# Kernel tuning notes

Hardware: AMD Instinct MI355X
Metric: run time of the kernel (lower is better)

The kernel has to match this reference:

```python
import jax, jax.numpy as jnp
from jax import lax
import numpy as np

V, E, H = 32000, 32, 8  # vocab, embed dim, hidden dim
S, B = 128, 64          # seq_len, batch


def setup_inputs() -> dict:
    key = jax.random.key(0)
    ks = jax.random.split(key, 16)
    u = lambda k, shape, s: jax.random.uniform(k, shape, jnp.float32, -s, s)
    sH = 1.0 / np.sqrt(H)
    sE = 1.0 / np.sqrt(E)
    sV = 1.0 / np.sqrt(V)
    return {
        "input_batch": jax.random.randint(ks[0], (S, B), 0, V),
        "lookup": u(ks[1], (V, E), sE),
        "weight_xf": u(ks[2], (E, H), sH),
        "weight_hf": u(ks[3], (H, H), sH),
        "weight_xb": u(ks[4], (E, H), sH),
        "weight_hb": u(ks[5], (H, H), sH),
        "weight_o": u(ks[6], (2 * H, V), sV),
        "H_f": u(ks[7], (H,), sH),
        "H_b": u(ks[8], (H,), sH),
        "b_f1": u(ks[9], (H,), sH),
        "b_f2": u(ks[10], (H,), sH),
        "b_b1": u(ks[11], (H,), sH),
        "b_b2": u(ks[12], (H,), sH),
        "b_o": u(ks[13], (V,), sV),
    }


def reference(input_batch, lookup, weight_xf, weight_hf, weight_xb, weight_hb,
              weight_o, H_f, H_b, b_f1, b_f2, b_b1, b_b2, b_o):
    seq, bsz = input_batch.shape
    X = lookup[input_batch]  # [S, B, E]

    # NOTE: the torch code stores the hidden state BEFORE consuming token i
    # (H_f_table[i] = Hf_pre), so scan emits the carry before the update.
    def step_f(h, x):
        h_new = jnp.tanh(x @ weight_xf + b_f1 + h @ weight_hf + b_f2)
        return h_new, h

    def step_b(h, x):
        h_new = jnp.tanh(x @ weight_xb + b_b1 + h @ weight_hb + b_b2)
        return h_new, h

    h0f = jnp.broadcast_to(H_f, (bsz, H))
    h0b = jnp.broadcast_to(H_b, (bsz, H))
    _, Hf_table = lax.scan(step_f, h0f, X)            # [S, B, H] (pre-states)
    _, Hb_rev = lax.scan(step_b, h0b, X[::-1])        # reversed pre-states
    Hb_table = Hb_rev[::-1]                           # [S, B, H]

    Hcat = jnp.concatenate([Hf_table, Hb_table], axis=-1)   # [S, B, 2H]
    logits = jnp.einsum('sbh,hv->sbv', Hcat, weight_o) + b_o
    return jax.nn.log_softmax(logits, axis=-1)
```

## Files before the change

kernel.cpp:

```cpp
#include <hip/hip_runtime.h>

#define SEQ 128
#define BSZ 64
#define EMB 32
#define HD  8
#define VOC 32000
#define NPOS (SEQ * BSZ)
#define NRB  (NPOS / 32)
#define NVS  40
#define TPW  25

typedef float f32x4  __attribute__((ext_vector_type(4)));
typedef short bf16x8 __attribute__((ext_vector_type(8)));
typedef float f32x16 __attribute__((ext_vector_type(16)));

__device__ __forceinline__ unsigned short f2bf(float f) {
    union { float f; unsigned int u; } x; x.f = f;
    unsigned int r = x.u + 0x7fffu + ((x.u >> 16) & 1u);
    return (unsigned short)(r >> 16);
}

__global__ __launch_bounds__(256) void xproj_kernel(
    const int*   __restrict__ idx,
    const float* __restrict__ lookup,
    const float* __restrict__ Wxf, const float* __restrict__ Wxb,
    const float* __restrict__ bf1, const float* __restrict__ bf2,
    const float* __restrict__ bb1, const float* __restrict__ bb2,
    float* __restrict__ xpf, float* __restrict__ xpb)
{
    const int i = blockIdx.x * 256 + threadIdx.x;
    if (i >= NPOS) return;
    const int s = i >> 6;
    const int b = i & 63;

    const float* xr = lookup + (size_t)idx[i] * EMB;
    float x[EMB];
#pragma unroll
    for (int e = 0; e < EMB; ++e) x[e] = xr[e];

#pragma unroll
    for (int h = 0; h < HD; ++h) {
        float af = bf1[h] + bf2[h];
        float ab = bb1[h] + bb2[h];
#pragma unroll
        for (int e = 0; e < EMB; ++e) {
            af = fmaf(x[e], Wxf[e * HD + h], af);
            ab = fmaf(x[e], Wxb[e * HD + h], ab);
        }
        xpf[(b * HD + h) * SEQ + s]             = af;
        xpb[(b * HD + h) * SEQ + (SEQ - 1 - s)] = ab;
    }
}

__global__ __launch_bounds__(512) void rnn_scan_kernel(
    const float* __restrict__ xpf, const float* __restrict__ xpb,
    const float* __restrict__ Whf, const float* __restrict__ Whb,
    const float* __restrict__ Hf0, const float* __restrict__ Hb0,
    unsigned short* __restrict__ hc2)
{
    const int dir = blockIdx.x;
    const int tid = threadIdx.x;
    const int b   = tid >> 3;
    const int h   = tid & 7;

    const float* Wh = dir ? Whb : Whf;
    const float* xp = (dir ? xpb : xpf) + (size_t)tid * SEQ;

    float wh[HD];
#pragma unroll
    for (int j = 0; j < HD; ++j) wh[j] = Wh[j * HD + h];

    float xs[SEQ];
    const f32x4* xp4 = (const f32x4*)xp;
#pragma unroll
    for (int q = 0; q < SEQ / 4; ++q) {
        f32x4 v = xp4[q];
        xs[4 * q + 0] = v.x; xs[4 * q + 1] = v.y;
        xs[4 * q + 2] = v.z; xs[4 * q + 3] = v.w;
    }

    float hcur = dir ? Hb0[h] : Hf0[h];
    const int koff = dir ? HD : 0;

#pragma unroll
    for (int t = 0; t < SEQ; ++t) {
        const int s = dir ? (SEQ - 1 - t) : t;
        hc2[(s * BSZ + b) * 16 + koff + h] = f2bf(hcur);

        float acc = xs[t];
#pragma unroll
        for (int j = 0; j < HD; ++j)
            acc = fmaf(__shfl(hcur, j, 8), wh[j], acc);

        float e = __expf(2.0f * acc);
        hcur = (e - 1.0f) / (e + 1.0f);
    }
}

__global__ __launch_bounds__(256) void wo_prep_kernel(
    const float* __restrict__ Wo, unsigned short* __restrict__ wt)
{
    const int v = blockIdx.x * 256 + threadIdx.x;
    if (v >= VOC) return;
#pragma unroll
    for (int k = 0; k < 16; ++k)
        wt[v * 16 + k] = f2bf(Wo[k * VOC + v]);
}

__global__ __launch_bounds__(256) void lse_partial_kernel(
    const unsigned short* __restrict__ hc2,
    const unsigned short* __restrict__ wt,
    const float* __restrict__ bo,
    float* __restrict__ partial)
{
    const int gw   = blockIdx.x * 4 + (threadIdx.x >> 6);
    const int rb   = gw / NVS;
    const int vs   = gw - rb * NVS;
    const int lane = threadIdx.x & 63;
    const int half = lane >> 5;
    const int lc   = lane & 31;

    const bf16x8 afrag = *(const bf16x8*)(hc2 + (size_t)(rb * 32 + lc) * 16 + half * 8);

    f32x16 zv;
#pragma unroll
    for (int i = 0; i < 16; ++i) zv[i] = 0.0f;

    float sacc[16];
#pragma unroll
    for (int g = 0; g < 16; ++g) sacc[g] = 0.0f;

    for (int t = 0; t < TPW; ++t) {
        const int v0 = (vs * TPW + t) * 32;
        const bf16x8 bfrag = *(const bf16x8*)(wt + (size_t)(v0 + lc) * 16 + half * 8);
        f32x16 d = __builtin_amdgcn_mfma_f32_32x32x16_bf16(afrag, bfrag, zv, 0, 0, 0);
        const float bov = bo[v0 + lc];
#pragma unroll
        for (int g = 0; g < 16; ++g)
            sacc[g] += __expf(d[g] + bov);
    }

#pragma unroll
    for (int g = 0; g < 16; ++g) {
        float s = sacc[g];
        s += __shfl_xor(s, 1, 32);
        s += __shfl_xor(s, 2, 32);
        s += __shfl_xor(s, 4, 32);
        s += __shfl_xor(s, 8, 32);
        s += __shfl_xor(s, 16, 32);
        sacc[g] = s;
    }

    if (lc == 0) {
#pragma unroll
        for (int g = 0; g < 16; ++g) {
            const int row = (g & 3) + 8 * (g >> 2) + 4 * half;
            partial[(size_t)(rb * 32 + row) * NVS + vs] = sacc[g];
        }
    }
}

__global__ __launch_bounds__(256) void lse_reduce_kernel(
    const float* __restrict__ partial, float* __restrict__ lse)
{
    const int row = blockIdx.x * 256 + threadIdx.x;
    if (row >= NPOS) return;
    const f32x4* p4 = (const f32x4*)(partial + (size_t)row * NVS);
    float s = 0.0f;
#pragma unroll
    for (int q = 0; q < NVS / 4; ++q) {
        f32x4 v = p4[q];
        s += v.x + v.y + v.z + v.w;
    }
    lse[row] = logf(s);
}

__global__ __launch_bounds__(256) void out_mfma_kernel(
    const unsigned short* __restrict__ hc2,
    const unsigned short* __restrict__ wt,
    const float* __restrict__ bo,
    const float* __restrict__ lse,
    float* __restrict__ out)
{
    const int gw   = blockIdx.x * 4 + (threadIdx.x >> 6);
    const int rb   = gw / NVS;
    const int vs   = gw - rb * NVS;
    const int lane = threadIdx.x & 63;
    const int half = lane >> 5;
    const int lc   = lane & 31;

    const bf16x8 afrag = *(const bf16x8*)(hc2 + (size_t)(rb * 32 + lc) * 16 + half * 8);

    f32x16 zv;
#pragma unroll
    for (int i = 0; i < 16; ++i) zv[i] = 0.0f;

    float lse16[16];
#pragma unroll
    for (int g = 0; g < 16; ++g) {
        const int row = (g & 3) + 8 * (g >> 2) + 4 * half;
        lse16[g] = lse[rb * 32 + row];
    }

    for (int t = 0; t < TPW; ++t) {
        const int v0 = (vs * TPW + t) * 32;
        const bf16x8 bfrag = *(const bf16x8*)(wt + (size_t)(v0 + lc) * 16 + half * 8);
        f32x16 d = __builtin_amdgcn_mfma_f32_32x32x16_bf16(afrag, bfrag, zv, 0, 0, 0);
        const float bov = bo[v0 + lc];
#pragma unroll
        for (int g = 0; g < 16; ++g) {
            const int row = (g & 3) + 8 * (g >> 2) + 4 * half;
            const float val = d[g] + bov - lse16[g];
            __builtin_nontemporal_store(
                val, out + (size_t)(rb * 32 + row) * VOC + v0 + lc);
        }
    }
}

extern "C" void kernel_launch(void* const* d_in, const int* in_sizes, int n_in,
                              void* d_out, int out_size, void* d_ws, size_t ws_size,
                              hipStream_t stream)
{
    const int*   idx    = (const int*)  d_in[0];
    const float* lookup = (const float*)d_in[1];
    const float* Wxf    = (const float*)d_in[2];
    const float* Whf    = (const float*)d_in[3];
    const float* Wxb    = (const float*)d_in[4];
    const float* Whb    = (const float*)d_in[5];
    const float* Wo     = (const float*)d_in[6];
    const float* Hf0    = (const float*)d_in[7];
    const float* Hb0    = (const float*)d_in[8];
    const float* bf1    = (const float*)d_in[9];
    const float* bf2    = (const float*)d_in[10];
    const float* bb1    = (const float*)d_in[11];
    const float* bb2    = (const float*)d_in[12];
    const float* bo     = (const float*)d_in[13];
    float* out = (float*)d_out;

    char* ws = (char*)d_ws;
    float*          xpf     = (float*)ws;                    ws += BSZ * HD * SEQ * 4;
    float*          xpb     = (float*)ws;                    ws += BSZ * HD * SEQ * 4;
    unsigned short* hc2     = (unsigned short*)ws;           ws += NPOS * 16 * 2;
    unsigned short* wt      = (unsigned short*)ws;           ws += VOC * 16 * 2;
    float*          partial = (float*)ws;                    ws += (size_t)NPOS * NVS * 4;
    float*          lse     = (float*)ws;                    ws += NPOS * 4;

    hipLaunchKernelGGL(xproj_kernel, dim3(NPOS / 256), dim3(256), 0, stream,
                       idx, lookup, Wxf, Wxb, bf1, bf2, bb1, bb2, xpf, xpb);
    hipLaunchKernelGGL(wo_prep_kernel, dim3((VOC + 255) / 256), dim3(256), 0, stream,
                       Wo, wt);
    hipLaunchKernelGGL(rnn_scan_kernel, dim3(2), dim3(512), 0, stream,
                       xpf, xpb, Whf, Whb, Hf0, Hb0, hc2);
    hipLaunchKernelGGL(lse_partial_kernel, dim3(NRB * NVS / 4), dim3(256), 0, stream,
                       hc2, wt, bo, partial);
    hipLaunchKernelGGL(lse_reduce_kernel, dim3(NPOS / 256), dim3(256), 0, stream,
                       partial, lse);
    hipLaunchKernelGGL(out_mfma_kernel, dim3(NRB * NVS / 4), dim3(256), 0, stream,
                       hc2, wt, bo, lse, out);
}
```

Measured before the change: 292.0 us.

## Fuse prep kernels, fold LSE reduction into output kernel, use exp2 with prescaled weights

```diff
diff --git a/kernel.cpp b/kernel.cpp
--- a/kernel.cpp
+++ b/kernel.cpp
@@ -9,6 +9,7 @@
 #define NRB  (NPOS / 32)
 #define NVS  40
 #define TPW  25
+#define LOG2E 1.4426950408889634f
 
 typedef float f32x4  __attribute__((ext_vector_type(4)));
 typedef short bf16x8 __attribute__((ext_vector_type(8)));
@@ -20,35 +21,50 @@
     return (unsigned short)(r >> 16);
 }
 
-__global__ __launch_bounds__(256) void xproj_kernel(
+__global__ __launch_bounds__(256) void prep_kernel(
     const int*   __restrict__ idx,
     const float* __restrict__ lookup,
     const float* __restrict__ Wxf, const float* __restrict__ Wxb,
     const float* __restrict__ bf1, const float* __restrict__ bf2,
     const float* __restrict__ bb1, const float* __restrict__ bb2,
-    float* __restrict__ xpf, float* __restrict__ xpb)
-{
-    const int i = blockIdx.x * 256 + threadIdx.x;
-    if (i >= NPOS) return;
-    const int s = i >> 6;
-    const int b = i & 63;
-
-    const float* xr = lookup + (size_t)idx[i] * EMB;
-    float x[EMB];
-#pragma unroll
-    for (int e = 0; e < EMB; ++e) x[e] = xr[e];
-
-#pragma unroll
-    for (int h = 0; h < HD; ++h) {
-        float af = bf1[h] + bf2[h];
-        float ab = bb1[h] + bb2[h];
-#pragma unroll
-        for (int e = 0; e < EMB; ++e) {
-            af = fmaf(x[e], Wxf[e * HD + h], af);
-            ab = fmaf(x[e], Wxb[e * HD + h], ab);
-        }
-        xpf[(b * HD + h) * SEQ + s]             = af;
-        xpb[(b * HD + h) * SEQ + (SEQ - 1 - s)] = ab;
+    const float* __restrict__ Wo,  const float* __restrict__ bo,
+    float* __restrict__ xpf, float* __restrict__ xpb,
+    unsigned short* __restrict__ wt, unsigned short* __restrict__ wt2,
+    float* __restrict__ bo2)
+{
+    if (blockIdx.x < 32) {
+        const int i = blockIdx.x * 256 + threadIdx.x;
+        const int s = i >> 6;
+        const int b = i & 63;
+
+        const float* xr = lookup + (size_t)idx[i] * EMB;
+        float x[EMB];
+#pragma unroll
+        for (int e = 0; e < EMB; ++e) x[e] = xr[e];
+
+#pragma unroll
+        for (int h = 0; h < HD; ++h) {
+            float af = bf1[h] + bf2[h];
+            float ab = bb1[h] + bb2[h];
+#pragma unroll
+            for (int e = 0; e < EMB; ++e) {
+                af = fmaf(x[e], Wxf[e * HD + h], af);
+                ab = fmaf(x[e], Wxb[e * HD + h], ab);
+            }
+            xpf[(b * HD + h) * SEQ + s]             = af;
+            xpb[(b * HD + h) * SEQ + (SEQ - 1 - s)] = ab;
+        }
+    } else {
+        const int v = (blockIdx.x - 32) * 256 + threadIdx.x;
+        if (v < VOC) {
+#pragma unroll
+            for (int k = 0; k < 16; ++k) {
+                const float w = Wo[k * VOC + v];
+                wt [v * 16 + k] = f2bf(w);
+                wt2[v * 16 + k] = f2bf(w * LOG2E);
+            }
+            bo2[v] = bo[v] * LOG2E;
+        }
     }
 }
 
@@ -97,20 +113,10 @@
     }
 }
 
-__global__ __launch_bounds__(256) void wo_prep_kernel(
-    const float* __restrict__ Wo, unsigned short* __restrict__ wt)
-{
-    const int v = blockIdx.x * 256 + threadIdx.x;
-    if (v >= VOC) return;
-#pragma unroll
-    for (int k = 0; k < 16; ++k)
-        wt[v * 16 + k] = f2bf(Wo[k * VOC + v]);
-}
-
 __global__ __launch_bounds__(256) void lse_partial_kernel(
     const unsigned short* __restrict__ hc2,
-    const unsigned short* __restrict__ wt,
-    const float* __restrict__ bo,
+    const unsigned short* __restrict__ wt2,
+    const float* __restrict__ bo2,
     float* __restrict__ partial)
 {
     const int gw   = blockIdx.x * 4 + (threadIdx.x >> 6);
@@ -132,12 +138,12 @@
 
     for (int t = 0; t < TPW; ++t) {
         const int v0 = (vs * TPW + t) * 32;
-        const bf16x8 bfrag = *(const bf16x8*)(wt + (size_t)(v0 + lc) * 16 + half * 8);
+        const bf16x8 bfrag = *(const bf16x8*)(wt2 + (size_t)(v0 + lc) * 16 + half * 8);
         f32x16 d = __builtin_amdgcn_mfma_f32_32x32x16_bf16(afrag, bfrag, zv, 0, 0, 0);
-        const float bov = bo[v0 + lc];
+        const float bov = bo2[v0 + lc];
 #pragma unroll
         for (int g = 0; g < 16; ++g)
-            sacc[g] += __expf(d[g] + bov);
+            sacc[g] += exp2f(d[g] + bov);
     }
 
 #pragma unroll
@@ -160,26 +166,11 @@
     }
 }
 
-__global__ __launch_bounds__(256) void lse_reduce_kernel(
-    const float* __restrict__ partial, float* __restrict__ lse)
-{
-    const int row = blockIdx.x * 256 + threadIdx.x;
-    if (row >= NPOS) return;
-    const f32x4* p4 = (const f32x4*)(partial + (size_t)row * NVS);
-    float s = 0.0f;
-#pragma unroll
-    for (int q = 0; q < NVS / 4; ++q) {
-        f32x4 v = p4[q];
-        s += v.x + v.y + v.z + v.w;
-    }
-    lse[row] = logf(s);
-}
-
 __global__ __launch_bounds__(256) void out_mfma_kernel(
     const unsigned short* __restrict__ hc2,
     const unsigned short* __restrict__ wt,
     const float* __restrict__ bo,
-    const float* __restrict__ lse,
+    const float* __restrict__ partial,
     float* __restrict__ out)
 {
     const int gw   = blockIdx.x * 4 + (threadIdx.x >> 6);
@@ -189,18 +180,29 @@
     const int half = lane >> 5;
     const int lc   = lane & 31;
 
-    const bf16x8 afrag = *(const bf16x8*)(hc2 + (size_t)(rb * 32 + lc) * 16 + half * 8);
-
-    f32x16 zv;
-#pragma unroll
-    for (int i = 0; i < 16; ++i) zv[i] = 0.0f;
+    const float* pbase = partial + (size_t)rb * 32 * NVS
+                       + (lane >> 1) * NVS + (lane & 1) * (NVS / 2);
+    float s = 0.0f;
+    const f32x4* p4 = (const f32x4*)pbase;
+#pragma unroll
+    for (int q = 0; q < NVS / 8; ++q) {
+        f32x4 v = p4[q];
+        s += v.x + v.y + v.z + v.w;
+    }
+    s += __shfl_xor(s, 1, 64);
 
     float lse16[16];
 #pragma unroll
     for (int g = 0; g < 16; ++g) {
         const int row = (g & 3) + 8 * (g >> 2) + 4 * half;
-        lse16[g] = lse[rb * 32 + row];
-    }
+        lse16[g] = logf(__shfl(s, 2 * row, 64));
+    }
+
+    const bf16x8 afrag = *(const bf16x8*)(hc2 + (size_t)(rb * 32 + lc) * 16 + half * 8);
+
+    f32x16 zv;
+#pragma unroll
+    for (int i = 0; i < 16; ++i) zv[i] = 0.0f;
 
     for (int t = 0; t < TPW; ++t) {
         const int v0 = (vs * TPW + t) * 32;
@@ -238,23 +240,21 @@
     float* out = (float*)d_out;
 
     char* ws = (char*)d_ws;
-    float*          xpf     = (float*)ws;                    ws += BSZ * HD * SEQ * 4;
-    float*          xpb     = (float*)ws;                    ws += BSZ * HD * SEQ * 4;
-    unsigned short* hc2     = (unsigned short*)ws;           ws += NPOS * 16 * 2;
-    unsigned short* wt      = (unsigned short*)ws;           ws += VOC * 16 * 2;
-    float*          partial = (float*)ws;                    ws += (size_t)NPOS * NVS * 4;
-    float*          lse     = (float*)ws;                    ws += NPOS * 4;
-
-    hipLaunchKernelGGL(xproj_kernel, dim3(NPOS / 256), dim3(256), 0, stream,
-                       idx, lookup, Wxf, Wxb, bf1, bf2, bb1, bb2, xpf, xpb);
-    hipLaunchKernelGGL(wo_prep_kernel, dim3((VOC + 255) / 256), dim3(256), 0, stream,
-                       Wo, wt);
+    float*          xpf     = (float*)ws;          ws += BSZ * HD * SEQ * 4;
+    float*          xpb     = (float*)ws;          ws += BSZ * HD * SEQ * 4;
+    unsigned short* hc2     = (unsigned short*)ws; ws += NPOS * 16 * 2;
+    unsigned short* wt      = (unsigned short*)ws; ws += VOC * 16 * 2;
+    unsigned short* wt2     = (unsigned short*)ws; ws += VOC * 16 * 2;
+    float*          bo2     = (float*)ws;          ws += VOC * 4;
+    float*          partial = (float*)ws;          ws += (size_t)NPOS * NVS * 4;
+
+    hipLaunchKernelGGL(prep_kernel, dim3(32 + (VOC + 255) / 256), dim3(256), 0, stream,
+                       idx, lookup, Wxf, Wxb, bf1, bf2, bb1, bb2, Wo, bo,
+                       xpf, xpb, wt, wt2, bo2);
     hipLaunchKernelGGL(rnn_scan_kernel, dim3(2), dim3(512), 0, stream,
                        xpf, xpb, Whf, Whb, Hf0, Hb0, hc2);
     hipLaunchKernelGGL(lse_partial_kernel, dim3(NRB * NVS / 4), dim3(256), 0, stream,
-                       hc2, wt, bo, partial);
-    hipLaunchKernelGGL(lse_reduce_kernel, dim3(NPOS / 256), dim3(256), 0, stream,
-                       partial, lse);
+                       hc2, wt2, bo2, partial);
     hipLaunchKernelGGL(out_mfma_kernel, dim3(NRB * NVS / 4), dim3(256), 0, stream,
-                       hc2, wt, bo, lse, out);
-}
+                       hc2, wt, bo, partial, out);
+}
```

After: 314.8 us. +7.8%, slower.
